# Kernel optimization log

Measured on AMD Instinct MI355X. Metric: run time of the kernel, lower is better.

Reference implementation:

```python
import jax, jax.numpy as jnp
import numpy as np
import math

B, S, D = 1, 4096, 512
H, KVH, DH = 8, 4, 64
DH2 = DH // 2
M = int(math.isqrt(S))           # product-key grid side, S == M*M
K = 8                            # top_k
ROPE_BASE = 10000.0


def rope_cos_sin(seq_len, dh, base):
    inv_freq = 1.0 / (base ** (jnp.arange(0, dh, 2, dtype=jnp.float32) / dh))
    t = jnp.arange(seq_len, dtype=jnp.float32)
    freqs = jnp.outer(t, inv_freq)                      # (S, dh/2)
    emb = jnp.concatenate([freqs, freqs], axis=-1)      # (S, dh)
    return jnp.cos(emb), jnp.sin(emb)


def apply_rope(x, cos, sin):
    # x: (B, H, S, dh); half-split rotation (llama-style)
    dh2 = x.shape[-1] // 2
    rot = jnp.concatenate([-x[..., dh2:], x[..., :dh2]], axis=-1)
    return x * cos + rot * sin


def setup_inputs() -> dict:
    key = jax.random.key(0)
    ks = jax.random.split(key, 5)
    s = 0.02
    x = jax.random.normal(ks[0], (B, S, D), dtype=jnp.float32)
    Wq = jax.random.normal(ks[1], (H * DH, D), dtype=jnp.float32) * s
    Wk = jax.random.normal(ks[2], (KVH * DH, D), dtype=jnp.float32) * s
    Wv = jax.random.normal(ks[3], (KVH * DH, D), dtype=jnp.float32) * s
    Wo = jax.random.normal(ks[4], (D, H * DH), dtype=jnp.float32) * s
    return {"x": x, "Wq": Wq, "Wk": Wk, "Wv": Wv, "Wo": Wo}


def reference(x, Wq, Wk, Wv, Wo):
    b, s, d = x.shape
    cos, sin = rope_cos_sin(s, DH, ROPE_BASE)
    q = (x @ Wq.T).reshape(b, s, H, DH).transpose(0, 2, 1, 3)      # (B,H,S,DH)
    k = (x @ Wk.T).reshape(b, s, KVH, DH).transpose(0, 2, 1, 3)    # (B,KVH,S,DH)
    v = (x @ Wv.T).reshape(b, s, KVH, DH).transpose(0, 2, 1, 3)
    q = apply_rope(q, cos, sin)
    k = apply_rope(k, cos, sin)
    rep = H // KVH                                                 # GQA repeat_kv
    k = jnp.repeat(k, rep, axis=1)                                 # (B,H,S,DH)
    v = jnp.repeat(v, rep, axis=1)

    # factorized product keys: sum over grid rows / cols
    kg = k.reshape(b, H, M, M, DH)
    k1 = kg[..., :DH2].sum(axis=-2)                                # (B,H,M,DH2)
    k2 = kg[..., DH2:].sum(axis=-3)                                # (B,H,M,DH2)
    q1, q2 = q[..., :DH2], q[..., DH2:]

    def topk_sel(qh, kh):  # qh: (S,DH2), kh: (M,DH2)
        scores = qh @ kh.T                                         # (S,M)
        _, idx = jax.lax.top_k(scores, K)                          # (S,K)
        return kh[idx], idx                                        # (S,K,DH2), (S,K)

    sel2 = jax.vmap(jax.vmap(topk_sel))
    k1v, i1 = sel2(q1, k1)                                         # (B,H,S,K,DH2)
    k2v, i2 = sel2(q2, k2)

    # cross-product candidates: (B,H,S,K,K,DH) -> (B,H,S,K*K,DH)
    c1 = jnp.broadcast_to(k1v[:, :, :, :, None, :], (b, H, s, K, K, DH2))
    c2 = jnp.broadcast_to(k2v[:, :, :, None, :, :], (b, H, s, K, K, DH2))
    cand = jnp.concatenate([c1, c2], axis=-1).reshape(b, H, s, K * K, DH)

    scores_final = jnp.einsum('bhsd,bhscd->bhsc', q, cand)         # (B,H,S,K*K)
    _, sel = jax.lax.top_k(scores_final, K)                        # (B,H,S,K)
    final_k = jnp.take_along_axis(cand, sel[..., None], axis=3)    # (B,H,S,K,DH)

    row = jnp.take_along_axis(i1, sel // K, axis=3)
    col = jnp.take_along_axis(i2, sel % K, axis=3)
    v_idx = row * M + col                                          # (B,H,S,K)
    final_v = jax.vmap(jax.vmap(lambda vb, ib: vb[ib]))(v, v_idx)  # (B,H,S,K,DH)

    attn = jax.nn.softmax(
        jnp.einsum('bhsd,bhskd->bhsk', q, final_k) / math.sqrt(DH), axis=-1)
    o = jnp.einsum('bhsk,bhskd->bhsd', attn, final_v)              # (B,H,S,DH)
    o = o.transpose(0, 2, 1, 3).reshape(b, s, H * DH)
    return o @ Wo.T
```

## Files before the change

kernel.cpp:

```cpp
#include <hip/hip_runtime.h>
#include <math.h>


static constexpr size_t OFF_QKV = 0;
static constexpr size_t OFF_Q   = 4194304;
static constexpr size_t OFF_K   = 6291456;
static constexpr size_t OFF_V   = 7340032;
static constexpr size_t OFF_COS = 8388608;
static constexpr size_t OFF_SIN = 8519680;
static constexpr size_t OFF_K1  = 8650752;
static constexpr size_t OFF_K2  = 8658944;
static constexpr size_t OFF_O   = 8667136;
static constexpr size_t OFF_W   = 10764288;

#define LDB 132

__device__ __forceinline__ float rdlane_f(float v, int lane) {
  return __int_as_float(__builtin_amdgcn_readlane(__float_as_int(v), lane));
}

__global__ __launch_bounds__(256) void freq_table_kernel(float* __restrict__ cosT,
    float* __restrict__ sinT) {
  int idx = blockIdx.x * 256 + threadIdx.x;
  int s = idx >> 5;
  int dp = idx & 31;
  double e = (double)dp * (1.0 / 32.0);
  float pf = (float)pow(10000.0, e);
  float invf = 1.0f / pf;
  float argf = __fmul_rn((float)s, invf);
  cosT[idx] = (float)cos((double)argf);
  sinT[idx] = (float)sin((double)argf);
}

template <int SPLIT>
__global__ __launch_bounds__(256) void gemm128_chain(const float* __restrict__ A,
    const float* __restrict__ B, float* __restrict__ C, int N) {
  __shared__ float As[16 * LDB];
  __shared__ float Bs[16 * LDB];
  const int tid = threadIdx.x;
  const int bm = blockIdx.y, bn = blockIdx.x;
  const int lrow = tid >> 1;
  const int lko = (tid & 1) << 3;
  const int ty = tid >> 4;
  const int tx = tid & 15;
  const float* Ap = A + (size_t)(bm * 128 + lrow) * 512 + lko;
  const float* Bp = B + (size_t)(bn * 128 + lrow) * 512 + lko;
  float acc1[8][8] = {{0.f}};
  float acc2[8][8] = {{0.f}};
  float4 a0 = *(const float4*)(Ap + 0);
  float4 a1 = *(const float4*)(Ap + 4);
  float4 b0 = *(const float4*)(Bp + 0);
  float4 b1 = *(const float4*)(Bp + 4);
  for (int kt = 0; kt < 512; kt += 16) {
    __syncthreads();
    As[(lko + 0) * LDB + lrow] = a0.x;
    As[(lko + 1) * LDB + lrow] = a0.y;
    As[(lko + 2) * LDB + lrow] = a0.z;
    As[(lko + 3) * LDB + lrow] = a0.w;
    As[(lko + 4) * LDB + lrow] = a1.x;
    As[(lko + 5) * LDB + lrow] = a1.y;
    As[(lko + 6) * LDB + lrow] = a1.z;
    As[(lko + 7) * LDB + lrow] = a1.w;
    Bs[(lko + 0) * LDB + lrow] = b0.x;
    Bs[(lko + 1) * LDB + lrow] = b0.y;
    Bs[(lko + 2) * LDB + lrow] = b0.z;
    Bs[(lko + 3) * LDB + lrow] = b0.w;
    Bs[(lko + 4) * LDB + lrow] = b1.x;
    Bs[(lko + 5) * LDB + lrow] = b1.y;
    Bs[(lko + 6) * LDB + lrow] = b1.z;
    Bs[(lko + 7) * LDB + lrow] = b1.w;
    __syncthreads();
    if (kt + 16 < 512) {
      a0 = *(const float4*)(Ap + kt + 16);
      a1 = *(const float4*)(Ap + kt + 20);
      b0 = *(const float4*)(Bp + kt + 16);
      b1 = *(const float4*)(Bp + kt + 20);
    }
    if (SPLIT != 0 && kt >= SPLIT) {
      #pragma unroll
      for (int k = 0; k < 16; ++k) {
        float4 al = *(const float4*)(&As[k * LDB + (ty << 3)]);
        float4 ah = *(const float4*)(&As[k * LDB + (ty << 3) + 4]);
        float4 bl = *(const float4*)(&Bs[k * LDB + (tx << 3)]);
        float4 bh = *(const float4*)(&Bs[k * LDB + (tx << 3) + 4]);
        float af[8] = {al.x, al.y, al.z, al.w, ah.x, ah.y, ah.z, ah.w};
        float bf[8] = {bl.x, bl.y, bl.z, bl.w, bh.x, bh.y, bh.z, bh.w};
        #pragma unroll
        for (int i2 = 0; i2 < 8; ++i2)
          #pragma unroll
          for (int j2 = 0; j2 < 8; ++j2)
            acc2[i2][j2] = fmaf(af[i2], bf[j2], acc2[i2][j2]);
      }
    } else {
      #pragma unroll
      for (int k = 0; k < 16; ++k) {
        float4 al = *(const float4*)(&As[k * LDB + (ty << 3)]);
        float4 ah = *(const float4*)(&As[k * LDB + (ty << 3) + 4]);
        float4 bl = *(const float4*)(&Bs[k * LDB + (tx << 3)]);
        float4 bh = *(const float4*)(&Bs[k * LDB + (tx << 3) + 4]);
        float af[8] = {al.x, al.y, al.z, al.w, ah.x, ah.y, ah.z, ah.w};
        float bf[8] = {bl.x, bl.y, bl.z, bl.w, bh.x, bh.y, bh.z, bh.w};
        #pragma unroll
        for (int i2 = 0; i2 < 8; ++i2)
          #pragma unroll
          for (int j2 = 0; j2 < 8; ++j2)
            acc1[i2][j2] = fmaf(af[i2], bf[j2], acc1[i2][j2]);
      }
    }
  }
  #pragma unroll
  for (int i2 = 0; i2 < 8; ++i2) {
    float* Cp = C + (size_t)(bm * 128 + (ty << 3) + i2) * N + bn * 128 + (tx << 3);
    float4 lo, hi;
    if (SPLIT != 0) {
      lo.x = __fadd_rn(acc1[i2][0], acc2[i2][0]);
      lo.y = __fadd_rn(acc1[i2][1], acc2[i2][1]);
      lo.z = __fadd_rn(acc1[i2][2], acc2[i2][2]);
      lo.w = __fadd_rn(acc1[i2][3], acc2[i2][3]);
      hi.x = __fadd_rn(acc1[i2][4], acc2[i2][4]);
      hi.y = __fadd_rn(acc1[i2][5], acc2[i2][5]);
      hi.z = __fadd_rn(acc1[i2][6], acc2[i2][6]);
      hi.w = __fadd_rn(acc1[i2][7], acc2[i2][7]);
    } else {
      lo = make_float4(acc1[i2][0], acc1[i2][1], acc1[i2][2], acc1[i2][3]);
      hi = make_float4(acc1[i2][4], acc1[i2][5], acc1[i2][6], acc1[i2][7]);
    }
    *(float4*)(Cp)     = lo;
    *(float4*)(Cp + 4) = hi;
  }
}

__global__ __launch_bounds__(256) void rope_reshape_kernel(const float* __restrict__ raw,
    const float* __restrict__ cosT, const float* __restrict__ sinT,
    float* __restrict__ qb, float* __restrict__ kb, float* __restrict__ vb) {
  int idx = blockIdx.x * 256 + threadIdx.x;
  int s = idx >> 10;
  int n = idx & 1023;
  float val = raw[idx];
  int d = n & 63;
  if (n < 768) {
    int dp = d & 31;
    float cs = cosT[(s << 5) + dp];
    float sn = sinT[(s << 5) + dp];
    int npart = (n - d) + ((d < 32) ? d + 32 : d - 32);
    float partner = raw[(s << 10) + npart];
    float rot = (d < 32) ? -partner : partner;
    float out = __fadd_rn(__fmul_rn(val, cs), __fmul_rn(rot, sn));
    if (n < 512) {
      int h = n >> 6;
      qb[((size_t)(h * 4096 + s) << 6) + d] = out;
    } else {
      int kvh = (n - 512) >> 6;
      kb[((size_t)(kvh * 4096 + s) << 6) + d] = out;
    }
  } else {
    int kvh = (n - 768) >> 6;
    vb[((size_t)(kvh * 4096 + s) << 6) + d] = val;
  }
}

__global__ __launch_bounds__(256) void k12_np_kernel(const float* __restrict__ kb,
    float* __restrict__ k1t, float* __restrict__ k2t) {
  int id = blockIdx.x * 256 + threadIdx.x;
  int which = id >> 13;
  int rem = id & 8191;
  int kvh = rem >> 11;
  int rem2 = rem & 2047;
  int i = rem2 >> 5;
  int d = rem2 & 31;
  const float* base = kb + ((size_t)(kvh * 4096) << 6);
  if (which == 0) {
    float acc = base[((size_t)(i * 64) << 6) + d];
    for (int c = 1; c < 64; ++c)
      acc = __fadd_rn(acc, base[((size_t)(i * 64 + c) << 6) + d]);
    k1t[(kvh * 64 + i) * 32 + d] = acc;
  } else {
    float acc = base[((size_t)i << 6) + d + 32];
    for (int r = 1; r < 64; ++r)
      acc = __fadd_rn(acc, base[((size_t)(r * 64 + i) << 6) + d + 32]);
    k2t[(kvh * 64 + i) * 32 + d] = acc;
  }
}

__global__ __launch_bounds__(256) void stage1_scores_kernel(
    const float* __restrict__ qb, const float* __restrict__ k1t,
    const float* __restrict__ k2t, float* __restrict__ sc) {
  __shared__ float qs[64 * 68];
  __shared__ float kd[32 * 132];
  const int t = threadIdx.x;
  const int h = blockIdx.y;
  const int s0 = blockIdx.x * 64;
  const int kvh = h >> 1;
  #pragma unroll
  for (int i = 0; i < 16; ++i) {
    int j = t + i * 256;
    int ss = j >> 6, d = j & 63;
    qs[d * 68 + ss] = qb[((size_t)(h * 4096 + s0 + ss) << 6) + d];
  }
  #pragma unroll
  for (int i = 0; i < 8; ++i) {
    int j = t + i * 256;
    int r = j >> 5, d = j & 31;
    kd[d * 132 + r]      = k1t[(kvh * 64 + r) * 32 + d];
    kd[d * 132 + 64 + r] = k2t[(kvh * 64 + r) * 32 + d];
  }
  __syncthreads();
  const int ty = t >> 4;
  const int tx = t & 15;
  const int qrow = (tx >= 8) ? 32 : 0;
  float acc[4][8] = {{0.f}};
  #pragma unroll
  for (int d = 0; d < 32; ++d) {
    float4 a4 = *(const float4*)&qs[(qrow + d) * 68 + (ty << 2)];
    float4 b0 = *(const float4*)&kd[d * 132 + (tx << 3)];
    float4 b1 = *(const float4*)&kd[d * 132 + (tx << 3) + 4];
    float af[4] = {a4.x, a4.y, a4.z, a4.w};
    float bf[8] = {b0.x, b0.y, b0.z, b0.w, b1.x, b1.y, b1.z, b1.w};
    #pragma unroll
    for (int i2 = 0; i2 < 4; ++i2)
      #pragma unroll
      for (int j2 = 0; j2 < 8; ++j2)
        acc[i2][j2] = fmaf(af[i2], bf[j2], acc[i2][j2]);
  }
  #pragma unroll
  for (int i2 = 0; i2 < 4; ++i2) {
    float* p = sc + (((size_t)(h * 4096 + s0 + (ty << 2) + i2)) << 7) + (tx << 3);
    *(float4*)(p)     = make_float4(acc[i2][0], acc[i2][1], acc[i2][2], acc[i2][3]);
    *(float4*)(p + 4) = make_float4(acc[i2][4], acc[i2][5], acc[i2][6], acc[i2][7]);
  }
}

__device__ __forceinline__ void bitonic64_val_desc(float& v, int lane) {
  #pragma unroll
  for (int k = 2; k <= 64; k <<= 1) {
    #pragma unroll
    for (int j = k >> 1; j >= 1; j >>= 1) {
      float ov = __shfl_xor(v, j, 64);
      bool up = ((lane & k) == 0) == ((lane & j) == 0);
      float mx = fmaxf(v, ov), mn = fminf(v, ov);
      v = up ? mx : mn;
    }
  }
}

__global__ __launch_bounds__(256) void attn_sel_kernel(const float* __restrict__ sc,
    const float* __restrict__ qb, const float* __restrict__ vb,
    const float* __restrict__ k1t, const float* __restrict__ k2t,
    float* __restrict__ ob) {
  const int lane = threadIdx.x & 63;
  const int w = blockIdx.x * 4 + (threadIdx.x >> 6);
  const int h = w >> 12;
  const int s = w & 4095;
  const int kvh = h >> 1;
  const float* scp = sc + ((size_t)w << 7);
  const float s1 = scp[lane];
  const float s2 = scp[64 + lane];
  const float qv = qb[((size_t)w << 6) + lane];

  float v1 = s1;
  bitonic64_val_desc(v1, lane);
  unsigned long long pack1 = 0, used = 0;
  #pragma unroll
  for (int t = 0; t < 8; ++t) {
    float tv = rdlane_f(v1, t);
    unsigned long long m = __ballot(s1 == tv) & ~used;
    int ix = __ffsll((long long)m) - 1;
    used |= 1ull << ix;
    pack1 |= (unsigned long long)ix << (6 * t);
  }
  float v2 = s2;
  bitonic64_val_desc(v2, lane);
  unsigned long long pack2 = 0;
  used = 0;
  #pragma unroll
  for (int t = 0; t < 8; ++t) {
    float tv = rdlane_f(v2, t);
    unsigned long long m = __ballot(s2 == tv) & ~used;
    int ix = __ffsll((long long)m) - 1;
    used |= 1ull << ix;
    pack2 |= (unsigned long long)ix << (6 * t);
  }

  int r1 = (int)((pack1 >> (6 * (lane >> 3))) & 63);
  int r2 = (int)((pack2 >> (6 * (lane & 7))) & 63);
  const float* k1p = k1t + (size_t)(kvh * 64 + r1) * 32;
  const float* k2p = k2t + (size_t)(kvh * 64 + r2) * 32;
  float c = 0.f;
  #pragma unroll
  for (int dq = 0; dq < 32; dq += 4) {
    float4 kk = *(const float4*)(k1p + dq);
    c = __fadd_rn(c, __fmul_rn(rdlane_f(qv, dq + 0), kk.x));
    c = __fadd_rn(c, __fmul_rn(rdlane_f(qv, dq + 1), kk.y));
    c = __fadd_rn(c, __fmul_rn(rdlane_f(qv, dq + 2), kk.z));
    c = __fadd_rn(c, __fmul_rn(rdlane_f(qv, dq + 3), kk.w));
  }
  #pragma unroll
  for (int dq = 0; dq < 32; dq += 4) {
    float4 kk = *(const float4*)(k2p + dq);
    c = __fadd_rn(c, __fmul_rn(rdlane_f(qv, 32 + dq + 0), kk.x));
    c = __fadd_rn(c, __fmul_rn(rdlane_f(qv, 32 + dq + 1), kk.y));
    c = __fadd_rn(c, __fmul_rn(rdlane_f(qv, 32 + dq + 2), kk.z));
    c = __fadd_rn(c, __fmul_rn(rdlane_f(qv, 32 + dq + 3), kk.w));
  }
  const float scand = c;
  float v3 = c;
  bitonic64_val_desc(v3, lane);
  float cvs[8]; int ccs[8];
  used = 0;
  #pragma unroll
  for (int t = 0; t < 8; ++t) {
    float tv = rdlane_f(v3, t);
    unsigned long long m = __ballot(scand == tv) & ~used;
    int ix = __ffsll((long long)m) - 1;
    used |= 1ull << ix;
    cvs[t] = tv;
    ccs[t] = ix;
  }
  float y[8];
  #pragma unroll
  for (int t = 0; t < 8; ++t) y[t] = cvs[t] * 0.125f;
  float mx = y[0];
  #pragma unroll
  for (int t = 1; t < 8; ++t) if (y[t] > mx) mx = y[t];
  float e[8];
  #pragma unroll
  for (int t = 0; t < 8; ++t) e[t] = __expf(__fsub_rn(y[t], mx));
  float wsum = __fadd_rn(__fadd_rn(__fadd_rn(e[0], e[1]), __fadd_rn(e[2], e[3])),
                         __fadd_rn(__fadd_rn(e[4], e[5]), __fadd_rn(e[6], e[7])));
  const float* vbh = vb + ((size_t)kvh << 18);
  float o = 0.f;
  #pragma unroll
  for (int t = 0; t < 8; ++t) {
    float att = __fdiv_rn(e[t], wsum);
    int row = (int)((pack1 >> (6 * (ccs[t] >> 3))) & 63);
    int col = (int)((pack2 >> (6 * (ccs[t] & 7))) & 63);
    o = __fadd_rn(o, __fmul_rn(att, vbh[((size_t)(row * 64 + col) << 6) + lane]));
  }
  ob[(size_t)s * 512 + (h << 6) + lane] = o;
}

extern "C" void kernel_launch(void* const* d_in, const int* in_sizes, int n_in,
                              void* d_out, int out_size, void* d_ws, size_t ws_size,
                              hipStream_t stream) {
  const float* x  = (const float*)d_in[0];
  const float* Wq = (const float*)d_in[1];
  const float* Wk = (const float*)d_in[2];
  const float* Wv = (const float*)d_in[3];
  const float* Wo = (const float*)d_in[4];
  float* ws = (float*)d_ws;
  float* qkv  = ws + OFF_QKV;
  float* qb   = ws + OFF_Q;
  float* kb   = ws + OFF_K;
  float* vb   = ws + OFF_V;
  float* cosT = ws + OFF_COS;
  float* sinT = ws + OFF_SIN;
  float* k1t  = ws + OFF_K1;
  float* k2t  = ws + OFF_K2;
  float* ob   = ws + OFF_O;
  float* wcat = ws + OFF_W;
  float* scb  = ws + OFF_QKV;

  hipMemcpyAsync(wcat,             Wq, (size_t)512 * 512 * sizeof(float), hipMemcpyDeviceToDevice, stream);
  hipMemcpyAsync(wcat + 512 * 512, Wk, (size_t)256 * 512 * sizeof(float), hipMemcpyDeviceToDevice, stream);
  hipMemcpyAsync(wcat + 768 * 512, Wv, (size_t)256 * 512 * sizeof(float), hipMemcpyDeviceToDevice, stream);

  freq_table_kernel<<<512, 256, 0, stream>>>(cosT, sinT);
  gemm128_chain<384><<<dim3(1024 / 128, 4096 / 128), 256, 0, stream>>>(x, wcat, qkv, 1024);
  rope_reshape_kernel<<<16384, 256, 0, stream>>>(qkv, cosT, sinT, qb, kb, vb);
  k12_np_kernel<<<64, 256, 0, stream>>>(kb, k1t, k2t);
  stage1_scores_kernel<<<dim3(64, 8), 256, 0, stream>>>(qb, k1t, k2t, scb);
  attn_sel_kernel<<<8192, 256, 0, stream>>>(scb, qb, vb, k1t, k2t, ob);
  gemm128_chain<0><<<dim3(512 / 128, 4096 / 128), 256, 0, stream>>>(ob, Wo, (float*)d_out, 512);
}
```

Before: 278.4 us.

## Split GEMM K dimension across grid z and merge partial sums downstream

Both projection GEMMs now split the K reduction across two blocks via blockIdx.z, each writing a partial output buffer. The QKV partial sums are added inside the RoPE reshape kernel, and the output projection gets a separate combine kernel. The shared-memory read pattern also changes to strided 4-wide fragments, which should reduce bank conflicts. This doubles the block count for better occupancy on the small grids, at the cost of extra partial-buffer traffic and one extra launch.

Result: faster. 244.7 us (-12.1%).

```diff
diff --git a/kernel.cpp b/kernel.cpp
--- a/kernel.cpp
+++ b/kernel.cpp
@@ -2,16 +2,17 @@
 #include <math.h>
 
 
-static constexpr size_t OFF_QKV = 0;
-static constexpr size_t OFF_Q   = 4194304;
-static constexpr size_t OFF_K   = 6291456;
-static constexpr size_t OFF_V   = 7340032;
-static constexpr size_t OFF_COS = 8388608;
-static constexpr size_t OFF_SIN = 8519680;
-static constexpr size_t OFF_K1  = 8650752;
-static constexpr size_t OFF_K2  = 8658944;
-static constexpr size_t OFF_O   = 8667136;
-static constexpr size_t OFF_W   = 10764288;
+static constexpr size_t OFF_P1  = 0;
+static constexpr size_t OFF_P2  = 4194304;
+static constexpr size_t OFF_Q   = 8388608;
+static constexpr size_t OFF_K   = 10485760;
+static constexpr size_t OFF_V   = 11534336;
+static constexpr size_t OFF_COS = 12582912;
+static constexpr size_t OFF_SIN = 12713984;
+static constexpr size_t OFF_K1  = 12845056;
+static constexpr size_t OFF_K2  = 12853248;
+static constexpr size_t OFF_O   = 12861440;
+static constexpr size_t OFF_W   = 14958592;
 
 #define LDB 132
 
@@ -32,12 +33,16 @@
   sinT[idx] = (float)sin((double)argf);
 }
 
-template <int SPLIT>
-__global__ __launch_bounds__(256) void gemm128_chain(const float* __restrict__ A,
-    const float* __restrict__ B, float* __restrict__ C, int N) {
+__global__ __launch_bounds__(256) void gemm128_panel(const float* __restrict__ A,
+    const float* __restrict__ B, float* __restrict__ C1, float* __restrict__ C2,
+    int N, int ksplit) {
   __shared__ float As[16 * LDB];
   __shared__ float Bs[16 * LDB];
   const int tid = threadIdx.x;
+  const int z = blockIdx.z;
+  const int k0 = z ? ksplit : 0;
+  const int k1 = z ? 512 : ksplit;
+  float* __restrict__ C = z ? C2 : C1;
   const int bm = blockIdx.y, bn = blockIdx.x;
   const int lrow = tid >> 1;
   const int lko = (tid & 1) << 3;
@@ -45,13 +50,12 @@
   const int tx = tid & 15;
   const float* Ap = A + (size_t)(bm * 128 + lrow) * 512 + lko;
   const float* Bp = B + (size_t)(bn * 128 + lrow) * 512 + lko;
-  float acc1[8][8] = {{0.f}};
-  float acc2[8][8] = {{0.f}};
-  float4 a0 = *(const float4*)(Ap + 0);
-  float4 a1 = *(const float4*)(Ap + 4);
-  float4 b0 = *(const float4*)(Bp + 0);
-  float4 b1 = *(const float4*)(Bp + 4);
-  for (int kt = 0; kt < 512; kt += 16) {
+  float acc[8][8] = {{0.f}};
+  float4 a0 = *(const float4*)(Ap + k0);
+  float4 a1 = *(const float4*)(Ap + k0 + 4);
+  float4 b0 = *(const float4*)(Bp + k0);
+  float4 b1 = *(const float4*)(Bp + k0 + 4);
+  for (int kt = k0; kt < k1; kt += 16) {
     __syncthreads();
     As[(lko + 0) * LDB + lrow] = a0.x;
     As[(lko + 1) * LDB + lrow] = a0.y;
@@ -70,80 +74,58 @@
     Bs[(lko + 6) * LDB + lrow] = b1.z;
     Bs[(lko + 7) * LDB + lrow] = b1.w;
     __syncthreads();
-    if (kt + 16 < 512) {
+    if (kt + 16 < k1) {
       a0 = *(const float4*)(Ap + kt + 16);
       a1 = *(const float4*)(Ap + kt + 20);
       b0 = *(const float4*)(Bp + kt + 16);
       b1 = *(const float4*)(Bp + kt + 20);
     }
-    if (SPLIT != 0 && kt >= SPLIT) {
+    #pragma unroll
+    for (int k = 0; k < 16; ++k) {
+      float4 al = *(const float4*)(&As[k * LDB + (ty << 2)]);
+      float4 ah = *(const float4*)(&As[k * LDB + 64 + (ty << 2)]);
+      float4 bl = *(const float4*)(&Bs[k * LDB + (tx << 2)]);
+      float4 bh = *(const float4*)(&Bs[k * LDB + 64 + (tx << 2)]);
+      float af[8] = {al.x, al.y, al.z, al.w, ah.x, ah.y, ah.z, ah.w};
+      float bf[8] = {bl.x, bl.y, bl.z, bl.w, bh.x, bh.y, bh.z, bh.w};
       #pragma unroll
-      for (int k = 0; k < 16; ++k) {
-        float4 al = *(const float4*)(&As[k * LDB + (ty << 3)]);
-        float4 ah = *(const float4*)(&As[k * LDB + (ty << 3) + 4]);
-        float4 bl = *(const float4*)(&Bs[k * LDB + (tx << 3)]);
-        float4 bh = *(const float4*)(&Bs[k * LDB + (tx << 3) + 4]);
-        float af[8] = {al.x, al.y, al.z, al.w, ah.x, ah.y, ah.z, ah.w};
-        float bf[8] = {bl.x, bl.y, bl.z, bl.w, bh.x, bh.y, bh.z, bh.w};
+      for (int i2 = 0; i2 < 8; ++i2)
         #pragma unroll
-        for (int i2 = 0; i2 < 8; ++i2)
-          #pragma unroll
-          for (int j2 = 0; j2 < 8; ++j2)
-            acc2[i2][j2] = fmaf(af[i2], bf[j2], acc2[i2][j2]);
-      }
-    } else {
-      #pragma unroll
-      for (int k = 0; k < 16; ++k) {
-        float4 al = *(const float4*)(&As[k * LDB + (ty << 3)]);
-        float4 ah = *(const float4*)(&As[k * LDB + (ty << 3) + 4]);
-        float4 bl = *(const float4*)(&Bs[k * LDB + (tx << 3)]);
-        float4 bh = *(const float4*)(&Bs[k * LDB + (tx << 3) + 4]);
-        float af[8] = {al.x, al.y, al.z, al.w, ah.x, ah.y, ah.z, ah.w};
-        float bf[8] = {bl.x, bl.y, bl.z, bl.w, bh.x, bh.y, bh.z, bh.w};
-        #pragma unroll
-        for (int i2 = 0; i2 < 8; ++i2)
-          #pragma unroll
-          for (int j2 = 0; j2 < 8; ++j2)
-            acc1[i2][j2] = fmaf(af[i2], bf[j2], acc1[i2][j2]);
-      }
+        for (int j2 = 0; j2 < 8; ++j2)
+          acc[i2][j2] = fmaf(af[i2], bf[j2], acc[i2][j2]);
     }
   }
   #pragma unroll
   for (int i2 = 0; i2 < 8; ++i2) {
-    float* Cp = C + (size_t)(bm * 128 + (ty << 3) + i2) * N + bn * 128 + (tx << 3);
-    float4 lo, hi;
-    if (SPLIT != 0) {
-      lo.x = __fadd_rn(acc1[i2][0], acc2[i2][0]);
-      lo.y = __fadd_rn(acc1[i2][1], acc2[i2][1]);
-      lo.z = __fadd_rn(acc1[i2][2], acc2[i2][2]);
-      lo.w = __fadd_rn(acc1[i2][3], acc2[i2][3]);
-      hi.x = __fadd_rn(acc1[i2][4], acc2[i2][4]);
-      hi.y = __fadd_rn(acc1[i2][5], acc2[i2][5]);
-      hi.z = __fadd_rn(acc1[i2][6], acc2[i2][6]);
-      hi.w = __fadd_rn(acc1[i2][7], acc2[i2][7]);
-    } else {
-      lo = make_float4(acc1[i2][0], acc1[i2][1], acc1[i2][2], acc1[i2][3]);
-      hi = make_float4(acc1[i2][4], acc1[i2][5], acc1[i2][6], acc1[i2][7]);
-    }
-    *(float4*)(Cp)     = lo;
-    *(float4*)(Cp + 4) = hi;
-  }
-}
-
-__global__ __launch_bounds__(256) void rope_reshape_kernel(const float* __restrict__ raw,
-    const float* __restrict__ cosT, const float* __restrict__ sinT,
-    float* __restrict__ qb, float* __restrict__ kb, float* __restrict__ vb) {
+    int row = bm * 128 + ((i2 < 4) ? (ty << 2) + i2 : 64 + (ty << 2) + i2 - 4);
+    float* Cp = C + (size_t)row * N + bn * 128;
+    *(float4*)(Cp + (tx << 2))      = make_float4(acc[i2][0], acc[i2][1], acc[i2][2], acc[i2][3]);
+    *(float4*)(Cp + 64 + (tx << 2)) = make_float4(acc[i2][4], acc[i2][5], acc[i2][6], acc[i2][7]);
+  }
+}
+
+__global__ __launch_bounds__(256) void combine_kernel(const float* __restrict__ p1,
+    const float* __restrict__ p2, float* __restrict__ out) {
+  int i = blockIdx.x * 256 + threadIdx.x;
+  out[i] = __fadd_rn(p1[i], p2[i]);
+}
+
+__global__ __launch_bounds__(256) void rope_reshape_kernel(const float* __restrict__ p1,
+    const float* __restrict__ p2, const float* __restrict__ cosT,
+    const float* __restrict__ sinT, float* __restrict__ qb,
+    float* __restrict__ kb, float* __restrict__ vb) {
   int idx = blockIdx.x * 256 + threadIdx.x;
   int s = idx >> 10;
   int n = idx & 1023;
-  float val = raw[idx];
+  float val = __fadd_rn(p1[idx], p2[idx]);
   int d = n & 63;
   if (n < 768) {
     int dp = d & 31;
     float cs = cosT[(s << 5) + dp];
     float sn = sinT[(s << 5) + dp];
     int npart = (n - d) + ((d < 32) ? d + 32 : d - 32);
-    float partner = raw[(s << 10) + npart];
+    int pidx = (s << 10) + npart;
+    float partner = __fadd_rn(p1[pidx], p2[pidx]);
     float rot = (d < 32) ? -partner : partner;
     float out = __fadd_rn(__fmul_rn(val, cs), __fmul_rn(rot, sn));
     if (n < 512) {
@@ -348,7 +330,8 @@
   const float* Wv = (const float*)d_in[3];
   const float* Wo = (const float*)d_in[4];
   float* ws = (float*)d_ws;
-  float* qkv  = ws + OFF_QKV;
+  float* p1   = ws + OFF_P1;
+  float* p2   = ws + OFF_P2;
   float* qb   = ws + OFF_Q;
   float* kb   = ws + OFF_K;
   float* vb   = ws + OFF_V;
@@ -358,17 +341,20 @@
   float* k2t  = ws + OFF_K2;
   float* ob   = ws + OFF_O;
   float* wcat = ws + OFF_W;
-  float* scb  = ws + OFF_QKV;
+  float* scb  = ws + OFF_P1;
+  float* op1  = ws + OFF_P2;
+  float* op2  = ws + OFF_P2 + 2097152;
 
   hipMemcpyAsync(wcat,             Wq, (size_t)512 * 512 * sizeof(float), hipMemcpyDeviceToDevice, stream);
   hipMemcpyAsync(wcat + 512 * 512, Wk, (size_t)256 * 512 * sizeof(float), hipMemcpyDeviceToDevice, stream);
   hipMemcpyAsync(wcat + 768 * 512, Wv, (size_t)256 * 512 * sizeof(float), hipMemcpyDeviceToDevice, stream);
 
   freq_table_kernel<<<512, 256, 0, stream>>>(cosT, sinT);
-  gemm128_chain<384><<<dim3(1024 / 128, 4096 / 128), 256, 0, stream>>>(x, wcat, qkv, 1024);
-  rope_reshape_kernel<<<16384, 256, 0, stream>>>(qkv, cosT, sinT, qb, kb, vb);
+  gemm128_panel<<<dim3(8, 32, 2), 256, 0, stream>>>(x, wcat, p1, p2, 1024, 384);
+  rope_reshape_kernel<<<16384, 256, 0, stream>>>(p1, p2, cosT, sinT, qb, kb, vb);
   k12_np_kernel<<<64, 256, 0, stream>>>(kb, k1t, k2t);
   stage1_scores_kernel<<<dim3(64, 8), 256, 0, stream>>>(qb, k1t, k2t, scb);
   attn_sel_kernel<<<8192, 256, 0, stream>>>(scb, qb, vb, k1t, k2t, ob);
-  gemm128_chain<0><<<dim3(512 / 128, 4096 / 128), 256, 0, stream>>>(ob, Wo, (float*)d_out, 512);
-}
+  gemm128_panel<<<dim3(4, 32, 2), 256, 0, stream>>>(ob, Wo, op1, op2, 512, 256);
+  combine_kernel<<<8192, 256, 0, stream>>>(op1, op2, (float*)d_out);
+}
```
